# Kernel optimization log

Hardware: AMD Instinct MI355X
Metric: run time of the kernel (lower is better)

## Reference

```python
import jax, jax.numpy as jnp
import numpy as np

LARGE_NEG = -1000000000.0
D_MODEL = 1024
NUM_HEADS = 16
DEPTH = D_MODEL // NUM_HEADS


def setup_inputs() -> dict:
    key = jax.random.key(0)
    ks = jax.random.split(key, 12)
    B, S, D = 4, 2048, D_MODEL
    scale = 1.0 / np.sqrt(D)
    inp = {
        "v": jax.random.normal(ks[0], (B, S, D), jnp.float32),
        "k": jax.random.normal(ks[1], (B, S, D), jnp.float32),
        "q": jax.random.normal(ks[2], (B, S, D), jnp.float32),
        "mask": jax.random.randint(ks[3], (B, 1, 1, S), 0, 2, jnp.int32),
        "Wq": jax.random.normal(ks[4], (D, D), jnp.float32) * scale,
        "bq": jnp.zeros((D,), jnp.float32),
        "Wk": jax.random.normal(ks[5], (D, D), jnp.float32) * scale,
        "bk": jnp.zeros((D,), jnp.float32),
        "Wv": jax.random.normal(ks[6], (D, D), jnp.float32) * scale,
        "bv": jnp.zeros((D,), jnp.float32),
        "Wo": jax.random.normal(ks[7], (D, D), jnp.float32) * scale,
        "bo": jnp.zeros((D,), jnp.float32),
    }
    return inp


def _split_heads(x):
    # [B, S, D] -> [B, H, S, depth]
    B, S, _ = x.shape
    return x.reshape(B, S, NUM_HEADS, DEPTH).transpose(0, 2, 1, 3)


def reference(v, k, q, mask, Wq, bq, Wk, bk, Wv, bv, Wo, bo):
    B, Sq, D = q.shape
    qh = _split_heads(q @ Wq + bq)  # [B,H,Sq,d]
    kh = _split_heads(k @ Wk + bk)  # [B,H,Sk,d]
    vh = _split_heads(v @ Wv + bv)  # [B,H,Sk,d]
    logits = jnp.einsum('bhqd,bhkd->bhqk', qh, kh) / jnp.sqrt(
        jnp.asarray(DEPTH, jnp.float32))
    logits = logits + mask.astype(jnp.float32) * LARGE_NEG
    attn = jax.nn.softmax(logits, axis=-1)
    ctx = jnp.einsum('bhqk,bhkd->bhqd', attn, vh)
    ctx = ctx.transpose(0, 2, 1, 3).reshape(B, Sq, D)  # concat heads
    return ctx @ Wo + bo
```

## Files before the change

### kernel.cpp

```cpp
#include <hip/hip_runtime.h>


typedef unsigned short ushort_t;
typedef __bf16          b16x8 __attribute__((ext_vector_type(8)));
typedef unsigned short  u16x8 __attribute__((ext_vector_type(8)));
typedef unsigned short  u16x4 __attribute__((ext_vector_type(4)));
typedef unsigned int    u32x4 __attribute__((ext_vector_type(4)));
typedef float           f32x4 __attribute__((ext_vector_type(4)));

#define B_ 4
#define S_ 2048
#define D_ 1024
#define H_ 16
#define DEPTH_ 64
#define LOG2E 1.4426950408889634f
#define MASKC (-1.4426950408889634e9f)

__device__ __forceinline__ unsigned short f2bf(float f) {
  unsigned u = __builtin_bit_cast(unsigned, f);
  u += 0x7FFFu + ((u >> 16) & 1u);
  return (unsigned short)(u >> 16);
}

__device__ __forceinline__ unsigned pack_trunc(float lo, float hi) {
#if __has_builtin(__builtin_amdgcn_perm)
  return __builtin_amdgcn_perm(__builtin_bit_cast(unsigned, hi),
                               __builtin_bit_cast(unsigned, lo), 0x07060302u);
#else
  return (__builtin_bit_cast(unsigned, hi) & 0xFFFF0000u) |
         (__builtin_bit_cast(unsigned, lo) >> 16);
#endif
}

#if __has_builtin(__builtin_amdgcn_exp2f)
#define EXP2F(x) __builtin_amdgcn_exp2f(x)
#else
#define EXP2F(x) exp2f(x)
#endif

#define GLD16(gp, lp) __builtin_amdgcn_global_load_lds( \
    (__attribute__((address_space(1))) void*)(gp),       \
    (__attribute__((address_space(3))) void*)(lp), 16, 0, 0)

#define MFMA_BF16(a, b, c) __builtin_amdgcn_mfma_f32_16x16x32_bf16( \
    __builtin_bit_cast(b16x8, (a)), __builtin_bit_cast(b16x8, (b)), (c), 0, 0, 0)


__global__ void cvt_kernel(const float* __restrict__ q, const float* __restrict__ k,
                           const float* __restrict__ v,
                           const float* __restrict__ Wq, const float* __restrict__ Wk,
                           const float* __restrict__ Wv, const float* __restrict__ Wo,
                           ushort_t* __restrict__ qb, ushort_t* __restrict__ kb,
                           ushort_t* __restrict__ vb,
                           ushort_t* __restrict__ Wqt, ushort_t* __restrict__ Wkt,
                           ushort_t* __restrict__ Wvt, ushort_t* __restrict__ Wot) {
  __shared__ float t[32][33];
  const int y = blockIdx.y;
  if (y < 3) {
    const float* src = y == 0 ? q : y == 1 ? k : v;
    ushort_t*    dst = y == 0 ? qb : y == 1 ? kb : vb;
    size_t i = ((size_t)blockIdx.x * 256 + threadIdx.x) * 4;
    float4 f = *(const float4*)(src + i);
    u16x4 o;
    o[0] = f2bf(f.x); o[1] = f2bf(f.y); o[2] = f2bf(f.z); o[3] = f2bf(f.w);
    *(u16x4*)(dst + i) = o;
    return;
  }
  const int x = blockIdx.x;
  if (x >= 4096) return;
  const int z = x >> 10, tile = x & 1023;
  const float* W = z == 0 ? Wq : z == 1 ? Wk : z == 2 ? Wv : Wo;
  ushort_t*   Wt = z == 0 ? Wqt : z == 1 ? Wkt : z == 2 ? Wvt : Wot;
  const int xx = threadIdx.x & 31, y0 = threadIdx.x >> 5;
  const int kt = (tile & 31) * 32, nt = (tile >> 5) * 32;
#pragma unroll
  for (int r = 0; r < 4; r++) {
    int row = y0 + r * 8;
    t[row][xx] = W[(size_t)(kt + row) * D_ + nt + xx];
  }
  __syncthreads();
#pragma unroll
  for (int r = 0; r < 4; r++) {
    int row = y0 + r * 8;
    Wt[(size_t)(nt + row) * D_ + kt + xx] = f2bf(t[xx][row]);
  }
}


__device__ __forceinline__ void gemm_core(const ushort_t* __restrict__ A,
                                          const ushort_t* __restrict__ Bt,
                                          ushort_t* As, ushort_t* Bs,
                                          int tm, int tn, f32x4* acc) {
  const int tid = threadIdx.x;
  const int lane = tid & 63, wid = tid >> 6;
  const int wm = (wid >> 1) * 64, wn = (wid & 1) * 64;
  const int srow = lane >> 3;
  const int scol = ((lane & 7) ^ srow) * 8;
  const ushort_t* gA[4];
  const ushort_t* gB[4];
#pragma unroll
  for (int c = 0; c < 4; c++) {
    const int ch = wid * 4 + c;
    gA[c] = A  + (size_t)(tm + ch * 8 + srow) * D_ + scol;
    gB[c] = Bt + (size_t)(tn + ch * 8 + srow) * D_ + scol;
  }
  const int fr = lane & 15, fq = lane >> 4;
#pragma unroll
  for (int i = 0; i < 16; i++) acc[i] = f32x4{0.f, 0.f, 0.f, 0.f};
  for (int k0 = 0; k0 < D_; k0 += 64) {
    __syncthreads();
#pragma unroll
    for (int c = 0; c < 4; c++) {
      const int ch = wid * 4 + c;
      GLD16(gA[c] + k0, As + ch * 512);
      GLD16(gB[c] + k0, Bs + ch * 512);
    }
    __syncthreads();
#pragma unroll
    for (int kh = 0; kh < 2; kh++) {
      const int coff = (((kh * 4 + fq) ^ (fr & 7))) * 8;
      u16x8 af[4], bf[4];
#pragma unroll
      for (int mi = 0; mi < 4; mi++)
        af[mi] = *(const u16x8*)(As + (wm + mi * 16 + fr) * 64 + coff);
#pragma unroll
      for (int ni = 0; ni < 4; ni++)
        bf[ni] = *(const u16x8*)(Bs + (wn + ni * 16 + fr) * 64 + coff);
#pragma unroll
      for (int mi = 0; mi < 4; mi++)
#pragma unroll
        for (int ni = 0; ni < 4; ni++)
          acc[mi * 4 + ni] = MFMA_BF16(af[mi], bf[ni], acc[mi * 4 + ni]);
    }
  }
}

__device__ __forceinline__ int sigma32(int k5) {
  return ((k5 & 15) >> 2) * 8 + ((k5 >> 4) & 1) * 4 + (k5 & 3);
}

__device__ __forceinline__ void gemm_tile_swizzle(int bx, int& tm, int& tn) {
  const int xcd = bx & 7, j = bx >> 3;
  tn = (j & 7) * 128;
  tm = (((j >> 3) << 3) | xcd) * 128;
}

__global__ __launch_bounds__(256, 3) void qkv_gemm_kernel(
    const ushort_t* __restrict__ qb, const ushort_t* __restrict__ kb, const ushort_t* __restrict__ vb,
    const ushort_t* __restrict__ Wqt, const ushort_t* __restrict__ Wkt, const ushort_t* __restrict__ Wvt,
    const float* __restrict__ bq, const float* __restrict__ bk, const float* __restrict__ bv,
    ushort_t* __restrict__ Qh, ushort_t* __restrict__ Kh, ushort_t* __restrict__ Vht) {
  __shared__ __align__(16) ushort_t smem[128 * 136];
  ushort_t* As = smem;
  ushort_t* Bs = smem + 8192;
  const int z = blockIdx.z;
  const ushort_t* A  = z == 0 ? qb : z == 1 ? kb : vb;
  const ushort_t* Bt = z == 0 ? Wqt : z == 1 ? Wkt : Wvt;
  const float* bias  = z == 0 ? bq : z == 1 ? bk : bv;
  int tm, tn;
  gemm_tile_swizzle(blockIdx.x, tm, tn);
  f32x4 acc[16];
  gemm_core(A, Bt, As, Bs, tm, tn, acc);
  const int lane = threadIdx.x & 63, wid = threadIdx.x >> 6;
  const int wm = (wid >> 1) * 64, wn = (wid & 1) * 64;
  const int fr = lane & 15, rq = (lane >> 4) * 4;
  if (z == 2) {
    __syncthreads();
    ushort_t* trans = smem;
#pragma unroll
    for (int ni = 0; ni < 4; ni++) {
      const int n = wn + ni * 16 + fr;
      const float bb = bias[tn + n];
#pragma unroll
      for (int mi = 0; mi < 4; mi++) {
#pragma unroll
        for (int r = 0; r < 4; r++) {
          const int m = wm + mi * 16 + rq + r;
          const int mp = (m & ~31) + sigma32(m & 31);
          trans[n * 136 + mp] = f2bf(acc[mi * 4 + ni][r] + bb);
        }
      }
    }
    __syncthreads();
    const int n = threadIdx.x >> 1, hf = threadIdx.x & 1;
    const int col = tn + n, hh = col >> 6, dd = col & 63;
    const int bI = tm >> 11, sb = (tm & 2047) + hf * 64;
    ushort_t* dst = Vht + ((size_t)(bI * H_ + hh) * DEPTH_ + dd) * S_ + sb;
    const ushort_t* srcp = trans + n * 136 + hf * 64;
#pragma unroll
    for (int i = 0; i < 8; i++)
      *(u16x8*)(dst + i * 8) = *(const u16x8*)(srcp + i * 8);
  } else {
    ushort_t* outp = (z == 0) ? Qh : Kh;
    const float qscale = (z == 0) ? 0.125f * LOG2E : 1.0f;
#pragma unroll
    for (int ni = 0; ni < 4; ni++) {
      const int col = tn + wn + ni * 16 + fr;
      const float bb = bias[col];
      const int h = col >> 6, dd = col & 63;
#pragma unroll
      for (int mi = 0; mi < 4; mi++) {
#pragma unroll
        for (int r = 0; r < 4; r++) {
          const int m = tm + wm + mi * 16 + rq + r;
          const int b = m >> 11, s = m & 2047;
          outp[((size_t)(b * H_ + h) * S_ + s) * DEPTH_ + dd] =
              f2bf((acc[mi * 4 + ni][r] + bb) * qscale);
        }
      }
    }
  }
}

__global__ __launch_bounds__(256, 3) void out_gemm_kernel(
    const ushort_t* __restrict__ ctx, const ushort_t* __restrict__ Wot,
    const float* __restrict__ bo, float* __restrict__ out) {
  __shared__ __align__(16) ushort_t As[8192], Bs[8192];
  int tm, tn;
  gemm_tile_swizzle(blockIdx.x, tm, tn);
  f32x4 acc[16];
  gemm_core(ctx, Wot, As, Bs, tm, tn, acc);
  const int lane = threadIdx.x & 63, wid = threadIdx.x >> 6;
  const int wm = (wid >> 1) * 64, wn = (wid & 1) * 64;
  const int fr = lane & 15, rq = (lane >> 4) * 4;
#pragma unroll
  for (int ni = 0; ni < 4; ni++) {
    const int col = tn + wn + ni * 16 + fr;
    const float bb = bo[col];
#pragma unroll
    for (int mi = 0; mi < 4; mi++) {
#pragma unroll
      for (int r = 0; r < 4; r++) {
        const int m = tm + wm + mi * 16 + rq + r;
        out[(size_t)m * D_ + col] = acc[mi * 4 + ni][r] + bb;
      }
    }
  }
}


__global__ __launch_bounds__(256, 4) void attn_kernel(
    const ushort_t* __restrict__ Qh, const ushort_t* __restrict__ Kh,
    const ushort_t* __restrict__ Vht, const int* __restrict__ mask,
    ushort_t* __restrict__ ctx) {
  __shared__ __align__(16) ushort_t Ks[128 * 64];
  __shared__ __align__(16) ushort_t Vs[64 * 128];
  __shared__ __align__(16) float Cm[2048];
  const int tid = threadIdx.x, lane = tid & 63, wid = tid >> 6;
  const int id = blockIdx.x;
  const int xcd = id & 7, j = id >> 3;
  const int qt = j & 15;
  const int bh = xcd * 8 + (j >> 4);
  const int b = bh >> 4, h = bh & 15;
  const size_t base = (size_t)bh * (S_ * DEPTH_);
  const int fr = lane & 15, fq = lane >> 4;

  const int* mrow = mask + b * S_;
#pragma unroll
  for (int i = 0; i < 8; i++) {
    const int idx = tid + i * 256;
    Cm[idx] = mrow[idx] ? MASKC : 0.0f;
  }

  u16x8 qf[2][2];
#pragma unroll
  for (int nq = 0; nq < 2; nq++)
#pragma unroll
    for (int kc = 0; kc < 2; kc++)
      qf[nq][kc] = *(const u16x8*)(Qh + base +
          (size_t)(qt * 128 + wid * 32 + nq * 16 + fr) * DEPTH_ + kc * 32 + fq * 8);

  u16x8 ones_f;
  {
    const unsigned short o = (fr == 0) ? (unsigned short)0x3F80 : (unsigned short)0;
#pragma unroll
    for (int jj = 0; jj < 8; jj++) ones_f[jj] = o;
  }

  f32x4 Oa[4][2];
  f32x4 lacc[2];
#pragma unroll
  for (int di = 0; di < 4; di++)
#pragma unroll
    for (int nq = 0; nq < 2; nq++) Oa[di][nq] = f32x4{0.f, 0.f, 0.f, 0.f};
#pragma unroll
  for (int nq = 0; nq < 2; nq++) lacc[nq] = f32x4{0.f, 0.f, 0.f, 0.f};

  const int krow = lane >> 3;
  const int kcolL = ((lane & 7) ^ (krow & 7)) * 8;
  const int vrowc = lane >> 4;
  const int koff0 = ((0 + fq) ^ (fr & 7)) * 8;
  const int koff1 = ((4 + fq) ^ (fr & 7)) * 8;

  for (int kt = 0; kt < 16; kt++) {
    __syncthreads();
#pragma unroll
    for (int c = 0; c < 4; c++) {
      const int ch = wid * 4 + c;
      GLD16(Kh + base + (size_t)(kt * 128 + ch * 8 + krow) * DEPTH_ + kcolL, Ks + ch * 512);
      const int vrow = ch * 4 + vrowc;
      const int vcolL = ((lane & 15) ^ (vrow & 15)) * 8;
      GLD16(Vht + base + (size_t)vrow * S_ + kt * 128 + vcolL, Vs + ch * 512);
    }
    __syncthreads();

#pragma unroll
    for (int ks = 0; ks < 4; ks++) {
      const int nk0 = ks * 2, nk1 = nk0 + 1;
      const ushort_t* kr0 = Ks + (nk0 * 16 + fr) * 64;
      const ushort_t* kr1 = Ks + (nk1 * 16 + fr) * 64;
      const u16x8 a00 = *(const u16x8*)(kr0 + koff0);
      const u16x8 a01 = *(const u16x8*)(kr0 + koff1);
      const u16x8 a10 = *(const u16x8*)(kr1 + koff0);
      const u16x8 a11 = *(const u16x8*)(kr1 + koff1);
      f32x4 st0[2], st1[2];
#pragma unroll
      for (int nq = 0; nq < 2; nq++) {
        f32x4 t = *(const f32x4*)(Cm + kt * 128 + nk0 * 16 + fq * 4);
        t = MFMA_BF16(a00, qf[nq][0], t);
        t = MFMA_BF16(a01, qf[nq][1], t);
        st0[nq] = t;
        f32x4 u = *(const f32x4*)(Cm + kt * 128 + nk1 * 16 + fq * 4);
        u = MFMA_BF16(a10, qf[nq][0], u);
        u = MFMA_BF16(a11, qf[nq][1], u);
        st1[nq] = u;
      }
      u16x8 pb[2];
#pragma unroll
      for (int nq = 0; nq < 2; nq++) {
#pragma unroll
        for (int r = 0; r < 4; r++) {
          st0[nq][r] = EXP2F(st0[nq][r]);
          st1[nq][r] = EXP2F(st1[nq][r]);
        }
        u32x4 pk;
        pk[0] = pack_trunc(st0[nq][0], st0[nq][1]);
        pk[1] = pack_trunc(st0[nq][2], st0[nq][3]);
        pk[2] = pack_trunc(st1[nq][0], st1[nq][1]);
        pk[3] = pack_trunc(st1[nq][2], st1[nq][3]);
        pb[nq] = __builtin_bit_cast(u16x8, pk);
      }
      const int voff = ((ks * 4 + fq) ^ fr) * 8;
#pragma unroll
      for (int di = 0; di < 4; di++) {
        const u16x8 vf = *(const u16x8*)(Vs + (di * 16 + fr) * 128 + voff);
#pragma unroll
        for (int nq = 0; nq < 2; nq++)
          Oa[di][nq] = MFMA_BF16(vf, pb[nq], Oa[di][nq]);
      }
#pragma unroll
      for (int nq = 0; nq < 2; nq++)
        lacc[nq] = MFMA_BF16(ones_f, pb[nq], lacc[nq]);
    }
  }

#pragma unroll
  for (int nq = 0; nq < 2; nq++) {
    const int lv = __builtin_amdgcn_ds_bpermute(fr * 4, __builtin_bit_cast(int, lacc[nq][0]));
    const float inv = 1.0f / __builtin_bit_cast(float, lv);
    const int sg = qt * 128 + wid * 32 + nq * 16 + fr;
    ushort_t* crow = ctx + ((size_t)(b * S_ + sg)) * D_ + h * DEPTH_;
#pragma unroll
    for (int di = 0; di < 4; di++) {
      u16x4 o4;
#pragma unroll
      for (int r = 0; r < 4; r++) o4[r] = f2bf(Oa[di][nq][r] * inv);
      *(u16x4*)(crow + di * 16 + fq * 4) = o4;
    }
  }
}


extern "C" void kernel_launch(void* const* d_in, const int* in_sizes, int n_in,
                              void* d_out, int out_size, void* d_ws, size_t ws_size,
                              hipStream_t stream) {
  const float* v  = (const float*)d_in[0];
  const float* k  = (const float*)d_in[1];
  const float* q  = (const float*)d_in[2];
  const int* mask = (const int*)d_in[3];
  const float* Wq = (const float*)d_in[4];
  const float* bq = (const float*)d_in[5];
  const float* Wk = (const float*)d_in[6];
  const float* bk = (const float*)d_in[7];
  const float* Wv = (const float*)d_in[8];
  const float* bv = (const float*)d_in[9];
  const float* Wo = (const float*)d_in[10];
  const float* bo = (const float*)d_in[11];
  float* out = (float*)d_out;

  char* ws = (char*)d_ws;
  ushort_t* qb  = (ushort_t*)(ws);
  ushort_t* kb  = (ushort_t*)(ws + (size_t)(16u << 20));
  ushort_t* vb  = (ushort_t*)(ws + (size_t)(32u << 20));
  ushort_t* Wqt = (ushort_t*)(ws + (size_t)(48u << 20));
  ushort_t* Wkt = (ushort_t*)(ws + (size_t)(50u << 20));
  ushort_t* Wvt = (ushort_t*)(ws + (size_t)(52u << 20));
  ushort_t* Wot = (ushort_t*)(ws + (size_t)(54u << 20));
  ushort_t* Qh  = (ushort_t*)(ws + (size_t)(56u << 20));
  ushort_t* Kh  = (ushort_t*)(ws + (size_t)(72u << 20));
  ushort_t* Vht = (ushort_t*)(ws + (size_t)(88u << 20));
  ushort_t* ctx = qb;

  cvt_kernel<<<dim3(8192, 4), 256, 0, stream>>>(q, k, v, Wq, Wk, Wv, Wo,
                                                qb, kb, vb, Wqt, Wkt, Wvt, Wot);
  qkv_gemm_kernel<<<dim3(512, 1, 3), 256, 0, stream>>>(qb, kb, vb, Wqt, Wkt, Wvt,
                                                       bq, bk, bv, Qh, Kh, Vht);
  attn_kernel<<<dim3(1024), 256, 0, stream>>>(Qh, Kh, Vht, mask, ctx);
  out_gemm_kernel<<<dim3(512), 256, 0, stream>>>(ctx, Wot, bo, out);
}
```

Measured before the change: 311.2 us.

## Fold key mask into zeroed V rows and masked row-sum instead of logit bias

Instead of adding a large negative bias to the logits, the QKV GEMM writes zeros into V for masked key positions. The attention kernel computes the softmax denominator with an MFMA against a per-key 0/1 mask vector, replacing the all-ones vector. This removes the per-tile float mask loads from LDS that seeded the score accumulators and halves the mask's LDS footprint. The trade-off is that masked keys now feed exp of unmasked, unnormalised logits into P, which relies on there being no max subtraction and on logits staying in a safe range.

```diff
diff --git a/kernel.cpp b/kernel.cpp
--- a/kernel.cpp
+++ b/kernel.cpp
@@ -14,7 +14,6 @@
 #define H_ 16
 #define DEPTH_ 64
 #define LOG2E 1.4426950408889634f
-#define MASKC (-1.4426950408889634e9f)
 
 __device__ __forceinline__ unsigned short f2bf(float f) {
   unsigned u = __builtin_bit_cast(unsigned, f);
@@ -149,8 +148,10 @@
     const ushort_t* __restrict__ qb, const ushort_t* __restrict__ kb, const ushort_t* __restrict__ vb,
     const ushort_t* __restrict__ Wqt, const ushort_t* __restrict__ Wkt, const ushort_t* __restrict__ Wvt,
     const float* __restrict__ bq, const float* __restrict__ bk, const float* __restrict__ bv,
+    const int* __restrict__ mask,
     ushort_t* __restrict__ Qh, ushort_t* __restrict__ Kh, ushort_t* __restrict__ Vht) {
   __shared__ __align__(16) ushort_t smem[128 * 136];
+  __shared__ int mloc[128];
   ushort_t* As = smem;
   ushort_t* Bs = smem + 8192;
   const int z = blockIdx.z;
@@ -165,6 +166,9 @@
   const int wm = (wid >> 1) * 64, wn = (wid & 1) * 64;
   const int fr = lane & 15, rq = (lane >> 4) * 4;
   if (z == 2) {
+    const int bI = tm >> 11;
+    if (threadIdx.x < 128)
+      mloc[threadIdx.x] = mask[bI * S_ + (tm & 2047) + threadIdx.x];
     __syncthreads();
     ushort_t* trans = smem;
 #pragma unroll
@@ -177,14 +181,14 @@
         for (int r = 0; r < 4; r++) {
           const int m = wm + mi * 16 + rq + r;
           const int mp = (m & ~31) + sigma32(m & 31);
-          trans[n * 136 + mp] = f2bf(acc[mi * 4 + ni][r] + bb);
+          trans[n * 136 + mp] = mloc[m] ? (unsigned short)0 : f2bf(acc[mi * 4 + ni][r] + bb);
         }
       }
     }
     __syncthreads();
     const int n = threadIdx.x >> 1, hf = threadIdx.x & 1;
     const int col = tn + n, hh = col >> 6, dd = col & 63;
-    const int bI = tm >> 11, sb = (tm & 2047) + hf * 64;
+    const int sb = (tm & 2047) + hf * 64;
     ushort_t* dst = Vht + ((size_t)(bI * H_ + hh) * DEPTH_ + dd) * S_ + sb;
     const ushort_t* srcp = trans + n * 136 + hf * 64;
 #pragma unroll
@@ -245,7 +249,7 @@
     ushort_t* __restrict__ ctx) {
   __shared__ __align__(16) ushort_t Ks[128 * 64];
   __shared__ __align__(16) ushort_t Vs[64 * 128];
-  __shared__ __align__(16) float Cm[2048];
+  __shared__ __align__(16) ushort_t Msk[2048];
   const int tid = threadIdx.x, lane = tid & 63, wid = tid >> 6;
   const int id = blockIdx.x;
   const int xcd = id & 7, j = id >> 3;
@@ -259,7 +263,8 @@
 #pragma unroll
   for (int i = 0; i < 8; i++) {
     const int idx = tid + i * 256;
-    Cm[idx] = mrow[idx] ? MASKC : 0.0f;
+    Msk[(idx & ~31) + sigma32(idx & 31)] =
+        mrow[idx] ? (unsigned short)0 : (unsigned short)0x3F80;
   }
 
   u16x8 qf[2][2];
@@ -270,12 +275,7 @@
       qf[nq][kc] = *(const u16x8*)(Qh + base +
           (size_t)(qt * 128 + wid * 32 + nq * 16 + fr) * DEPTH_ + kc * 32 + fq * 8);
 
-  u16x8 ones_f;
-  {
-    const unsigned short o = (fr == 0) ? (unsigned short)0x3F80 : (unsigned short)0;
-#pragma unroll
-    for (int jj = 0; jj < 8; jj++) ones_f[jj] = o;
-  }
+  const f32x4 zero4 = f32x4{0.f, 0.f, 0.f, 0.f};
 
   f32x4 Oa[4][2];
   f32x4 lacc[2];
@@ -313,15 +313,14 @@
       const u16x8 a01 = *(const u16x8*)(kr0 + koff1);
       const u16x8 a10 = *(const u16x8*)(kr1 + koff0);
       const u16x8 a11 = *(const u16x8*)(kr1 + koff1);
+      const u16x8 mf = *(const u16x8*)(Msk + kt * 128 + ks * 32 + fq * 8);
       f32x4 st0[2], st1[2];
 #pragma unroll
       for (int nq = 0; nq < 2; nq++) {
-        f32x4 t = *(const f32x4*)(Cm + kt * 128 + nk0 * 16 + fq * 4);
-        t = MFMA_BF16(a00, qf[nq][0], t);
+        f32x4 t = MFMA_BF16(a00, qf[nq][0], zero4);
         t = MFMA_BF16(a01, qf[nq][1], t);
         st0[nq] = t;
-        f32x4 u = *(const f32x4*)(Cm + kt * 128 + nk1 * 16 + fq * 4);
-        u = MFMA_BF16(a10, qf[nq][0], u);
+        f32x4 u = MFMA_BF16(a10, qf[nq][0], zero4);
         u = MFMA_BF16(a11, qf[nq][1], u);
         st1[nq] = u;
       }
@@ -350,7 +349,7 @@
       }
 #pragma unroll
       for (int nq = 0; nq < 2; nq++)
-        lacc[nq] = MFMA_BF16(ones_f, pb[nq], lacc[nq]);
+        lacc[nq] = MFMA_BF16(mf, pb[nq], lacc[nq]);
     }
   }
 
@@ -404,7 +403,7 @@
   cvt_kernel<<<dim3(8192, 4), 256, 0, stream>>>(q, k, v, Wq, Wk, Wv, Wo,
                                                 qb, kb, vb, Wqt, Wkt, Wvt, Wot);
   qkv_gemm_kernel<<<dim3(512, 1, 3), 256, 0, stream>>>(qb, kb, vb, Wqt, Wkt, Wvt,
-                                                       bq, bk, bv, Qh, Kh, Vht);
+                                                       bq, bk, bv, mask, Qh, Kh, Vht);
   attn_kernel<<<dim3(1024), 256, 0, stream>>>(Qh, Kh, Vht, mask, ctx);
   out_gemm_kernel<<<dim3(512), 256, 0, stream>>>(ctx, Wot, bo, out);
 }
```

Result: slower. 319.6 us (+2.7%).
